# Performance work log

Measured on AMD Instinct MI355X. Metric: run time of the kernel, lower is better.

The kernel has to match this reference:

```python
import jax, jax.numpy as jnp
import numpy as np


def setup_inputs() -> dict:
    key = jax.random.key(0)
    k1, k2, k3, k4, k5 = jax.random.split(key, 5)
    N, L, H = 512, 512, 768
    num_texts = 32
    hidden_states = jax.random.normal(k1, (N, L, H), dtype=jnp.float32)
    attention_mask = jax.random.randint(k2, (N, L), 0, 2).astype(jnp.int32)
    sample_map = jnp.sort(jax.random.randint(k3, (N,), 0, num_texts).astype(jnp.int64))
    Wq = jax.random.normal(k4, (H, H), dtype=jnp.float32) * (1.0 / np.sqrt(H))
    bq = jnp.zeros((H,), dtype=jnp.float32)
    Wk = jax.random.normal(k5, (H, H), dtype=jnp.float32) * (1.0 / np.sqrt(H))
    bk = jnp.zeros((H,), dtype=jnp.float32)
    return {
        'hidden_states': hidden_states,
        'attention_mask': attention_mask,
        'sample_map': sample_map,
        'Wq': Wq, 'bq': bq, 'Wk': Wk, 'bk': bk,
        'num_texts': num_texts,
    }


def _attn_pool(hidden_states, mask, Wq, bq, Wk, bk):
    # hidden_states: [N, L, H]; mask: [N, L]
    H = hidden_states.shape[-1]
    # Q from mean over sequence (unmasked mean, as in original)
    q = jnp.einsum('nh,oh->no', hidden_states.mean(axis=1), Wq) + bq   # [N, H]
    k = jnp.einsum('nlh,oh->nlo', hidden_states, Wk) + bk              # [N, L, H]
    scores = jnp.einsum('nh,nlh->nl', q, k) / jnp.sqrt(jnp.float32(H))  # [N, L]
    scores = jnp.where(mask == 0, jnp.float32(-1e9), scores)
    alphas = jax.nn.softmax(scores, axis=1)                            # [N, L]
    return jnp.einsum('nl,nlh->nh', alphas, hidden_states)             # [N, H]


def reference(hidden_states, attention_mask, sample_map, Wq, bq, Wk, bk, num_texts):
    # dropout is identity in eval mode
    pooled = _attn_pool(hidden_states, attention_mask, Wq, bq, Wk, bk)  # [N, H]
    seg = sample_map.astype(jnp.int32)
    sums = jax.ops.segment_sum(pooled, seg, num_segments=num_texts)     # [T, H]
    counts = jax.ops.segment_sum(jnp.ones((pooled.shape[0],), pooled.dtype), seg,
                                 num_segments=num_texts)                # [T]
    counts = jnp.clip(counts, 1.0, None)
    return sums / counts[:, None]
```

## Files before the change

kernel.cpp:

```cpp
#include <hip/hip_runtime.h>
#include <math.h>

#define HDIM 768
#define NG   192
#define LMAX 512

__device__ __forceinline__ float dot4(const float4 a, const float4 b) {
  return a.x * b.x + a.y * b.y + a.z * b.z + a.w * b.w;
}
__device__ __forceinline__ void fma4(float4& a, const float s, const float4 b) {
  a.x += s * b.x; a.y += s * b.y; a.z += s * b.z; a.w += s * b.w;
}
__device__ __forceinline__ void scale4(float4& a, const float s) {
  a.x *= s; a.y *= s; a.z *= s; a.w *= s;
}

__device__ __forceinline__ float wave_sum64(float x) {
  x += __int_as_float(__builtin_amdgcn_update_dpp(0, __float_as_int(x), 0xB1,  0xF, 0xF, true));
  x += __int_as_float(__builtin_amdgcn_update_dpp(0, __float_as_int(x), 0x4E,  0xF, 0xF, true));
  x += __int_as_float(__builtin_amdgcn_update_dpp(0, __float_as_int(x), 0x124, 0xF, 0xF, true));
  x += __int_as_float(__builtin_amdgcn_update_dpp(0, __float_as_int(x), 0x128, 0xF, 0xF, true));
  x += __int_as_float(__builtin_amdgcn_update_dpp(0, __float_as_int(x), 0x142, 0xF, 0xF, true));
  x += __int_as_float(__builtin_amdgcn_update_dpp(0, __float_as_int(x), 0x143, 0xF, 0xF, true));
  return __int_as_float(__builtin_amdgcn_readlane(__float_as_int(x), 63));
}

__global__ __launch_bounds__(256) void detect_slots(const unsigned* __restrict__ mask_w,
                                                    const unsigned* __restrict__ smap_w,
                                                    unsigned* __restrict__ slots,
                                                    int mask_words, int smap_words) {
  __shared__ unsigned red[2];
  const int b = blockIdx.x, tid = threadIdx.x;
  if (tid < 2) red[tid] = 0;
  __syncthreads();
  const int gtid = b * 256 + tid, gsz = gridDim.x * 256;
  unsigned acc = 0;
  for (int i = gtid; i < mask_words / 2; i += gsz) acc |= mask_w[2 * i + 1];
  unsigned acc2 = 0;
  for (int i = gtid; i < smap_words / 2; i += gsz) acc2 |= smap_w[2 * i + 1];
  if (acc)  atomicOr(&red[0], 1u);
  if (acc2) atomicOr(&red[1], 1u);
  __syncthreads();
  if (tid == 0) { slots[b] = red[0]; slots[64 + b] = red[1]; }
}

__global__ __launch_bounds__(256) void prep_wc(const float* __restrict__ Wq,
                                               const float* __restrict__ Wk,
                                               const float* __restrict__ bq,
                                               float* __restrict__ Wc,
                                               float* __restrict__ c0, int H) {
  __shared__ float As[16][33];
  __shared__ float Bs[16][65];
  __shared__ float bqs[16];
  const int i0 = blockIdx.x * 32, j0 = blockIdx.y * 64;
  const int idx = threadIdx.x;
  const int li = idx & 31, lk = idx >> 5;
  const int lj = idx & 63, lk2 = idx >> 6;
  const int tc = idx & 15, tr = idx >> 4;
  float c[2][4] = {{0.f,0.f,0.f,0.f},{0.f,0.f,0.f,0.f}};
  float cb[4] = {0.f,0.f,0.f,0.f};
  const bool bias_lane = (blockIdx.x == 0) && (tr == 0);
  for (int o0 = 0; o0 < H; o0 += 16) {
    __syncthreads();
    As[lk][li]       = Wq[(size_t)(o0 + lk) * H + i0 + li];
    As[lk + 8][li]   = Wq[(size_t)(o0 + lk + 8) * H + i0 + li];
    Bs[lk2][lj]      = Wk[(size_t)(o0 + lk2) * H + j0 + lj];
    Bs[lk2 + 4][lj]  = Wk[(size_t)(o0 + lk2 + 4) * H + j0 + lj];
    Bs[lk2 + 8][lj]  = Wk[(size_t)(o0 + lk2 + 8) * H + j0 + lj];
    Bs[lk2 + 12][lj] = Wk[(size_t)(o0 + lk2 + 12) * H + j0 + lj];
    if (idx < 16) bqs[idx] = bq[o0 + idx];
    __syncthreads();
#pragma unroll
    for (int k = 0; k < 16; ++k) {
      const float a0 = As[k][tr * 2], a1 = As[k][tr * 2 + 1];
      const float b0 = Bs[k][tc * 4],     b1 = Bs[k][tc * 4 + 1];
      const float b2 = Bs[k][tc * 4 + 2], b3 = Bs[k][tc * 4 + 3];
      c[0][0] += a0 * b0; c[0][1] += a0 * b1; c[0][2] += a0 * b2; c[0][3] += a0 * b3;
      c[1][0] += a1 * b0; c[1][1] += a1 * b1; c[1][2] += a1 * b2; c[1][3] += a1 * b3;
      if (bias_lane) {
        const float bv = bqs[k];
        cb[0] += bv * b0; cb[1] += bv * b1; cb[2] += bv * b2; cb[3] += bv * b3;
      }
    }
  }
#pragma unroll
  for (int j = 0; j < 4; ++j) {
    Wc[(size_t)(i0 + tr * 2) * H + j0 + tc * 4 + j]     = c[0][j];
    Wc[(size_t)(i0 + tr * 2 + 1) * H + j0 + tc * 4 + j] = c[1][j];
  }
  if (bias_lane) {
#pragma unroll
    for (int j = 0; j < 4; ++j) c0[j0 + tc * 4 + j] = cb[j];
  }
}

__global__ __launch_bounds__(384) void fused(const float* __restrict__ hs,
                                             const unsigned* __restrict__ mask_w,
                                             const float* __restrict__ Wc,
                                             const float* __restrict__ c0,
                                             const unsigned* __restrict__ slots,
                                             float* __restrict__ pooled, int L) {
  __shared__ float4 red2[NG];
  __shared__ float4 meanv4[NG];
  __shared__ float4 vv4[NG];
  __shared__ float4 redv4[6][NG];
  __shared__ float mw[6], sw[6];
  __shared__ int   mrow[LMAX];
  __shared__ int   vidx[LMAX];
  __shared__ int   nv_sh;
  __shared__ unsigned mfl;
  const int n = blockIdx.x, tid = threadIdx.x;
  const int w = tid >> 6, lane = tid & 63;

  if (tid == 0) mfl = 0u;
  __syncthreads();
  if (tid < 64 && slots[tid]) atomicOr(&mfl, 1u);

  const int half = tid / NG, t = tid - half * NG;
  const float4* hb = reinterpret_cast<const float4*>(hs) + (size_t)n * L * NG;
  float ax = 0.f, ay = 0.f, az = 0.f, aw = 0.f;
  int l = half;
  for (; l + 16 <= L; l += 16) {
    float4 u[8];
#pragma unroll
    for (int i = 0; i < 8; ++i) u[i] = hb[(size_t)(l + 2 * i) * NG + t];
#pragma unroll
    for (int i = 0; i < 8; ++i) { ax += u[i].x; ay += u[i].y; az += u[i].z; aw += u[i].w; }
  }
  for (; l < L; l += 2) {
    float4 u = hb[(size_t)l * NG + t];
    ax += u.x; ay += u.y; az += u.z; aw += u.w;
  }
  if (half == 1) { float4 o; o.x = ax; o.y = ay; o.z = az; o.w = aw; red2[t] = o; }
  __syncthreads();

  if (half == 0) {
    const float inv = 1.0f / (float)L;
    const float4 r = red2[t];
    float4 o;
    o.x = (ax + r.x) * inv; o.y = (ay + r.y) * inv;
    o.z = (az + r.z) * inv; o.w = (aw + r.w) * inv;
    meanv4[t] = o;
  }
  const int mask_is_i32 = (mfl != 0);
  for (int tt = tid; tt < L; tt += 384) {
    const size_t idx = (size_t)n * L + tt;
    mrow[tt] = (int)(mask_is_i32 ? mask_w[idx] : mask_w[2 * idx]);
  }
  __syncthreads();

  if (w == 0) {
    int off = 0;
    for (int seg = 0; seg < L; seg += 64) {
      const int mv = mrow[seg + lane];
      const unsigned long long bal = __ballot(mv != 0);
      const int rank = __popcll(bal & ((1ull << lane) - 1ull));
      if (mv != 0) vidx[off + rank] = seg + lane;
      off += __popcll(bal);
    }
    if (lane == 0) nv_sh = off;
  }

  {
    const int c1 = tid, c2 = tid + 384;
    float acc1 = 0.f, acc2 = 0.f;
    const float* wp = Wc;
    for (int o = 0; o < HDIM; o += 4) {
      const float4 mv = meanv4[o >> 2];
      acc1 += mv.x * wp[c1] + mv.y * wp[HDIM + c1] + mv.z * wp[2 * HDIM + c1] + mv.w * wp[3 * HDIM + c1];
      acc2 += mv.x * wp[c2] + mv.y * wp[HDIM + c2] + mv.z * wp[2 * HDIM + c2] + mv.w * wp[3 * HDIM + c2];
      wp += 4 * HDIM;
    }
    ((float*)vv4)[c1] = acc1 + c0[c1];
    ((float*)vv4)[c2] = acc2 + c0[c2];
  }
  __syncthreads();

  const int nv = nv_sh;
  if (nv == 0) {
#pragma unroll
    for (int part = 0; part < 2; ++part) {
      const int col = part * 384 + tid;
      pooled[(size_t)n * HDIM + col] = ((const float*)meanv4)[col];
    }
    return;
  }

  const float4 vf0 = vv4[lane], vf1 = vv4[64 + lane], vf2 = vv4[128 + lane];
  const float scale = 1.0f / sqrtf((float)HDIM);
  const int cntw = (nv > w) ? ((nv - 1 - w) / 6 + 1) : 0;
  const int cmax = (nv + 5) / 6;
  const int jmax = (cmax + 3) & ~3;
  const int vidx0 = vidx[0];
  float m = -3.0e38f, ss = 0.f;
  float4 A0 = {0,0,0,0}, A1 = {0,0,0,0}, A2 = {0,0,0,0};
  float4 xa[2][3], xb[2][3];

  auto ld = [&](float4 (&X)[2][3], int j) {
#pragma unroll
    for (int u = 0; u < 2; ++u) {
      const int jj = j + u;
      const int rr = (jj < cntw) ? vidx[6 * jj + w] : vidx0;
      const float4* rp = hb + (size_t)rr * NG;
      X[u][0] = rp[lane]; X[u][1] = rp[64 + lane]; X[u][2] = rp[128 + lane];
    }
  };
  auto pr = [&](float4 (&X)[2][3], int j) {
    float s[2];
#pragma unroll
    for (int u = 0; u < 2; ++u) {
      const float p = wave_sum64(dot4(X[u][0], vf0) + dot4(X[u][1], vf1) + dot4(X[u][2], vf2));
      s[u] = (j + u < cntw) ? p * scale : -3.0e38f;
    }
    const float mc = fmaxf(s[0], s[1]);
    if (mc > m) {
      const float f = __expf(m - mc);
      ss *= f; scale4(A0, f); scale4(A1, f); scale4(A2, f);
      m = mc;
    }
#pragma unroll
    for (int u = 0; u < 2; ++u) {
      const float pq = (j + u < cntw) ? __expf(s[u] - m) : 0.f;
      ss += pq;
      fma4(A0, pq, X[u][0]); fma4(A1, pq, X[u][1]); fma4(A2, pq, X[u][2]);
    }
  };

  ld(xa, 0);
  for (int j = 0; j < jmax; j += 4) {
    ld(xb, j + 2);
    pr(xa, j);
    if (j + 4 < jmax) ld(xa, j + 4);
    pr(xb, j + 2);
  }

  if (lane == 0) { mw[w] = m; sw[w] = ss; }
  redv4[w][lane]       = A0;
  redv4[w][64 + lane]  = A1;
  redv4[w][128 + lane] = A2;
  __syncthreads();
  float M = mw[0];
#pragma unroll
  for (int j = 1; j < 6; ++j) M = fmaxf(M, mw[j]);
  float f[6], S = 0.f;
#pragma unroll
  for (int j = 0; j < 6; ++j) { f[j] = __expf(mw[j] - M); S += sw[j] * f[j]; }
  const float invS = 1.0f / S;
  const float* redp = (const float*)redv4;
#pragma unroll
  for (int part = 0; part < 2; ++part) {
    const int col = part * 384 + tid;
    float o = 0.f;
#pragma unroll
    for (int j = 0; j < 6; ++j) o += redp[j * HDIM + col] * f[j];
    pooled[(size_t)n * HDIM + col] = o * invS;
  }
}

__global__ __launch_bounds__(256) void segmean(const float* __restrict__ pooled,
                                               const void* __restrict__ smap,
                                               const unsigned* __restrict__ slots_s,
                                               float* __restrict__ out, int N) {
  __shared__ unsigned fsh;
  const int t = blockIdx.x, tid = threadIdx.x;
  const int col = blockIdx.y * 256 + tid;
  if (tid == 0) {
    unsigned f = 0;
    for (int i = 0; i < 64; ++i) f |= slots_s[i];
    fsh = f;
  }
  __syncthreads();
  const int smap_is_i32 = (fsh != 0);
  float a = 0.f;
  int cnt = 0;
  for (int i = 0; i < N; ++i) {
    const int s = smap_is_i32 ? ((const int*)smap)[i]
                              : (int)((const long long*)smap)[i];
    if (s == t) { a += pooled[(size_t)i * HDIM + col]; ++cnt; }
  }
  out[(size_t)t * HDIM + col] = a / (float)(cnt > 0 ? cnt : 1);
}

extern "C" void kernel_launch(void* const* d_in, const int* in_sizes, int n_in,
                              void* d_out, int out_size, void* d_ws, size_t ws_size,
                              hipStream_t stream) {
  const float*    hs     = (const float*)d_in[0];
  const unsigned* mask_w = (const unsigned*)d_in[1];
  const void*     smap   = d_in[2];
  const float*    Wq     = (const float*)d_in[3];
  const float*    bq     = (const float*)d_in[4];
  const float*    Wk     = (const float*)d_in[5];

  const int N = in_sizes[2];
  const int L = in_sizes[1] / N;
  const int H = in_sizes[4];
  const int T = out_size / H;

  float* Wc     = (float*)d_ws;
  float* c0     = Wc + (size_t)H * H;
  float* pooled = c0 + H;
  unsigned* slots = (unsigned*)(pooled + (size_t)N * H);
  (void)ws_size; (void)n_in;

  detect_slots<<<64, 256, 0, stream>>>(mask_w, (const unsigned*)smap, slots, N * L, N);
  prep_wc<<<dim3(H / 32, H / 64), 256, 0, stream>>>(Wq, Wk, bq, Wc, c0, H);
  fused<<<N, 384, 0, stream>>>(hs, mask_w, Wc, c0, slots, pooled, L);
  segmean<<<dim3(T, 3), 256, 0, stream>>>(pooled, smap, slots + 64, (float*)d_out, N);
}
```

Measured before the change: 367.6 us.

## Split fused pool into compacting pass, batched GEMV, and fp16 softmax pass

Replaces the single fused per-sample kernel with a multi-stage pipeline when workspace allows. The first pass reads hidden states once, computes partial means and writes the mask-compacted valid rows as fp16. A separate batched GEMM then forms query vectors for all samples, and a second pass runs the online softmax over the compacted fp16 rows, split in two halves per sample and merged in segmean. This aims to avoid re-reading full fp32 hidden states and to increase parallelism, at the cost of extra launches, extra workspace traffic and fp16 rounding error in the scores and pooled values. It silently falls back to the old path if the workspace is too small, and the RCAP=256 per-half capacity assumes L/2 ≤ 256.

```diff
diff --git a/kernel.cpp b/kernel.cpp
--- a/kernel.cpp
+++ b/kernel.cpp
@@ -1,9 +1,11 @@
 #include <hip/hip_runtime.h>
+#include <hip/hip_fp16.h>
 #include <math.h>
 
 #define HDIM 768
 #define NG   192
 #define LMAX 512
+#define RCAP 256
 
 __device__ __forceinline__ float dot4(const float4 a, const float4 b) {
   return a.x * b.x + a.y * b.y + a.z * b.z + a.w * b.w;
@@ -13,6 +15,12 @@
 }
 __device__ __forceinline__ void scale4(float4& a, const float s) {
   a.x *= s; a.y *= s; a.z *= s; a.w *= s;
+}
+__device__ __forceinline__ float4 h8_to_f4(uint2 v) {
+  __half2 h0 = *reinterpret_cast<__half2*>(&v.x);
+  __half2 h1 = *reinterpret_cast<__half2*>(&v.y);
+  const float2 f0 = __half22float2(h0), f1 = __half22float2(h1);
+  return make_float4(f0.x, f0.y, f1.x, f1.y);
 }
 
 __device__ __forceinline__ float wave_sum64(float x) {
@@ -94,6 +102,253 @@
   }
 }
 
+__global__ __launch_bounds__(384) void passA(const float* __restrict__ hs,
+                                             const unsigned* __restrict__ mask_w,
+                                             const unsigned* __restrict__ slots,
+                                             float* __restrict__ part,
+                                             int* __restrict__ nvalid,
+                                             __half* __restrict__ hsc, int L) {
+  __shared__ float4 red2[NG];
+  __shared__ int cpos[RCAP];
+  __shared__ int mrow[RCAP];
+  __shared__ unsigned mfl;
+  const int bid = blockIdx.x, n = bid >> 1, half = bid & 1;
+  const int tid = threadIdx.x, lane = tid & 63;
+  const int Lh = L / 2, r0 = half * Lh;
+
+  if (tid == 0) mfl = 0u;
+  __syncthreads();
+  if (tid < 64 && slots[tid]) atomicOr(&mfl, 1u);
+  __syncthreads();
+  const int m32 = (mfl != 0);
+  if (tid < Lh) {
+    const size_t idx = (size_t)n * L + r0 + tid;
+    mrow[tid] = (int)(m32 ? mask_w[idx] : mask_w[2 * idx]);
+  }
+  __syncthreads();
+
+  int nv = 0;
+  for (int seg = 0; seg < Lh; seg += 64) {
+    const int mv = mrow[seg + lane];
+    const unsigned long long bal = __ballot(mv != 0);
+    const int rank = __popcll(bal & ((1ull << lane) - 1ull));
+    cpos[seg + lane] = (mv != 0) ? (nv + rank) : -1;
+    nv += __popcll(bal);
+  }
+
+  const int sub = tid / NG, t = tid - sub * NG;
+  const float4* hb = reinterpret_cast<const float4*>(hs) + ((size_t)n * L + r0) * NG;
+  __half* reg = hsc + (size_t)bid * (RCAP * HDIM);
+  float ax = 0.f, ay = 0.f, az = 0.f, aw = 0.f;
+
+  auto st16 = [&](const float4 u, int cp) {
+    __half2 h0 = __floats2half2_rn(u.x, u.y);
+    __half2 h1 = __floats2half2_rn(u.z, u.w);
+    uint2 pk;
+    pk.x = *reinterpret_cast<unsigned*>(&h0);
+    pk.y = *reinterpret_cast<unsigned*>(&h1);
+    reinterpret_cast<uint2*>(reg + (size_t)cp * HDIM)[t] = pk;
+  };
+
+  int l = sub;
+  for (; l + 16 <= Lh; l += 16) {
+    float4 u[8];
+#pragma unroll
+    for (int i = 0; i < 8; ++i) u[i] = hb[(size_t)(l + 2 * i) * NG + t];
+#pragma unroll
+    for (int i = 0; i < 8; ++i) { ax += u[i].x; ay += u[i].y; az += u[i].z; aw += u[i].w; }
+#pragma unroll
+    for (int i = 0; i < 8; ++i) {
+      const int cp = cpos[l + 2 * i];
+      if (cp >= 0) st16(u[i], cp);
+    }
+  }
+  for (; l < Lh; l += 2) {
+    const float4 u = hb[(size_t)l * NG + t];
+    ax += u.x; ay += u.y; az += u.z; aw += u.w;
+    const int cp = cpos[l];
+    if (cp >= 0) st16(u, cp);
+  }
+
+  if (sub == 1) { float4 o; o.x = ax; o.y = ay; o.z = az; o.w = aw; red2[t] = o; }
+  __syncthreads();
+  if (sub == 0) {
+    const float4 r = red2[t];
+    float4 o; o.x = ax + r.x; o.y = ay + r.y; o.z = az + r.z; o.w = aw + r.w;
+    reinterpret_cast<float4*>(part + (size_t)bid * HDIM)[t] = o;
+  }
+  if (tid == 0) nvalid[bid] = nv;
+}
+
+__global__ __launch_bounds__(256) void gemmV(const float* __restrict__ P,
+                                             const float* __restrict__ Wc,
+                                             const float* __restrict__ c0,
+                                             float* __restrict__ V,
+                                             int M, int Nn, int K, float invL) {
+  __shared__ float As[32][17];
+  __shared__ float Bs[16][65];
+  const int m0 = blockIdx.x * 32, n0 = blockIdx.y * 64;
+  const int idx = threadIdx.x;
+  const int lc = idx & 15, lr = idx >> 4;
+  const int bc = idx & 63, br = idx >> 6;
+  const int tc = idx & 15, tr = idx >> 4;
+  float c[2][4] = {{0.f,0.f,0.f,0.f},{0.f,0.f,0.f,0.f}};
+  for (int k0 = 0; k0 < K; k0 += 16) {
+    __syncthreads();
+    {
+      const int m1 = m0 + lr, m2 = m0 + lr + 16;
+      As[lr][lc]      = (P[(size_t)(2 * m1) * K + k0 + lc] + P[(size_t)(2 * m1 + 1) * K + k0 + lc]) * invL;
+      As[lr + 16][lc] = (P[(size_t)(2 * m2) * K + k0 + lc] + P[(size_t)(2 * m2 + 1) * K + k0 + lc]) * invL;
+    }
+    Bs[br][bc]      = Wc[(size_t)(k0 + br) * Nn + n0 + bc];
+    Bs[br + 4][bc]  = Wc[(size_t)(k0 + br + 4) * Nn + n0 + bc];
+    Bs[br + 8][bc]  = Wc[(size_t)(k0 + br + 8) * Nn + n0 + bc];
+    Bs[br + 12][bc] = Wc[(size_t)(k0 + br + 12) * Nn + n0 + bc];
+    __syncthreads();
+#pragma unroll
+    for (int k = 0; k < 16; ++k) {
+      const float a0 = As[tr * 2][k], a1 = As[tr * 2 + 1][k];
+      const float b0 = Bs[k][tc * 4], b1 = Bs[k][tc * 4 + 1];
+      const float b2 = Bs[k][tc * 4 + 2], b3 = Bs[k][tc * 4 + 3];
+      c[0][0] += a0 * b0; c[0][1] += a0 * b1; c[0][2] += a0 * b2; c[0][3] += a0 * b3;
+      c[1][0] += a1 * b0; c[1][1] += a1 * b1; c[1][2] += a1 * b2; c[1][3] += a1 * b3;
+    }
+  }
+#pragma unroll
+  for (int j = 0; j < 4; ++j) {
+    const float bv = c0[n0 + tc * 4 + j];
+    V[(size_t)(m0 + tr * 2) * Nn + n0 + tc * 4 + j]     = c[0][j] + bv;
+    V[(size_t)(m0 + tr * 2 + 1) * Nn + n0 + tc * 4 + j] = c[1][j] + bv;
+  }
+}
+
+__global__ __launch_bounds__(256) void poolc(const __half* __restrict__ hsc,
+                                             const int* __restrict__ nvalid,
+                                             const float* __restrict__ part,
+                                             const float* __restrict__ V,
+                                             float* __restrict__ acc_out,
+                                             float* __restrict__ ms_out, int L) {
+  __shared__ float4 redv[4][NG];
+  __shared__ float mw[4], sw[4];
+  const int bid = blockIdx.x, n = bid >> 1;
+  const int tid = threadIdx.x, w = tid >> 6, lane = tid & 63;
+  const int Lh = L / 2;
+  const int nv = nvalid[bid];
+
+  if (nv == 0) {
+#pragma unroll
+    for (int p = 0; p < 3; ++p) {
+      const int col = p * 256 + tid;
+      acc_out[(size_t)bid * HDIM + col] = part[(size_t)bid * HDIM + col];
+    }
+    if (tid == 0) { ms_out[bid * 2] = -1e9f; ms_out[bid * 2 + 1] = (float)Lh; }
+    return;
+  }
+
+  const float4* v4 = reinterpret_cast<const float4*>(V + (size_t)n * HDIM);
+  const float4 vf0 = v4[lane], vf1 = v4[64 + lane], vf2 = v4[128 + lane];
+  const uint2* rb = reinterpret_cast<const uint2*>(hsc + (size_t)bid * (RCAP * HDIM));
+  const float scale = 1.0f / sqrtf((float)HDIM);
+
+  const int cntw = (nv > w) ? ((nv - 1 - w) / 4 + 1) : 0;
+  const int cmax = (nv + 3) / 4;
+  const int jmax = (cmax + 3) & ~3;
+  float m = -3.0e38f, ss = 0.f;
+  float4 A0 = {0,0,0,0}, A1 = {0,0,0,0}, A2 = {0,0,0,0};
+  uint2 xa[2][3], xb[2][3];
+
+  auto ld = [&](uint2 (&X)[2][3], int j) {
+#pragma unroll
+    for (int u = 0; u < 2; ++u) {
+      const int jj = j + u;
+      const int rr = (jj < cntw) ? (4 * jj + w) : 0;
+      const uint2* rp = rb + (size_t)rr * NG;
+      X[u][0] = rp[lane]; X[u][1] = rp[64 + lane]; X[u][2] = rp[128 + lane];
+    }
+  };
+  auto pr = [&](uint2 (&X)[2][3], int j) {
+    float4 y[2][3];
+    float s[2];
+#pragma unroll
+    for (int u = 0; u < 2; ++u) {
+      y[u][0] = h8_to_f4(X[u][0]); y[u][1] = h8_to_f4(X[u][1]); y[u][2] = h8_to_f4(X[u][2]);
+      const float p = wave_sum64(dot4(y[u][0], vf0) + dot4(y[u][1], vf1) + dot4(y[u][2], vf2));
+      s[u] = (j + u < cntw) ? p * scale : -3.0e38f;
+    }
+    const float mc = fmaxf(s[0], s[1]);
+    if (mc > m) {
+      const float f = __expf(m - mc);
+      ss *= f; scale4(A0, f); scale4(A1, f); scale4(A2, f);
+      m = mc;
+    }
+#pragma unroll
+    for (int u = 0; u < 2; ++u) {
+      const float pq = (j + u < cntw) ? __expf(s[u] - m) : 0.f;
+      ss += pq;
+      fma4(A0, pq, y[u][0]); fma4(A1, pq, y[u][1]); fma4(A2, pq, y[u][2]);
+    }
+  };
+
+  ld(xa, 0);
+  for (int j = 0; j < jmax; j += 4) {
+    ld(xb, j + 2);
+    pr(xa, j);
+    if (j + 4 < jmax) ld(xa, j + 4);
+    pr(xb, j + 2);
+  }
+
+  if (lane == 0) { mw[w] = m; sw[w] = ss; }
+  redv[w][lane]       = A0;
+  redv[w][64 + lane]  = A1;
+  redv[w][128 + lane] = A2;
+  __syncthreads();
+  const float M = fmaxf(fmaxf(mw[0], mw[1]), fmaxf(mw[2], mw[3]));
+  const float f0 = __expf(mw[0] - M), f1 = __expf(mw[1] - M);
+  const float f2 = __expf(mw[2] - M), f3 = __expf(mw[3] - M);
+  const float S = sw[0] * f0 + sw[1] * f1 + sw[2] * f2 + sw[3] * f3;
+  const float* redp = (const float*)redv;
+#pragma unroll
+  for (int p = 0; p < 3; ++p) {
+    const int col = p * 256 + tid;
+    acc_out[(size_t)bid * HDIM + col] =
+        redp[col] * f0 + redp[HDIM + col] * f1 + redp[2 * HDIM + col] * f2 + redp[3 * HDIM + col] * f3;
+  }
+  if (tid == 0) { ms_out[bid * 2] = M; ms_out[bid * 2 + 1] = S; }
+}
+
+__global__ __launch_bounds__(256) void merge_segmean(const float* __restrict__ acc,
+                                                     const float* __restrict__ ms,
+                                                     const void* __restrict__ smap,
+                                                     const unsigned* __restrict__ slots_s,
+                                                     float* __restrict__ out, int N) {
+  __shared__ unsigned fsh;
+  const int t = blockIdx.x, tid = threadIdx.x;
+  const int col = blockIdx.y * 256 + tid;
+  if (tid == 0) {
+    unsigned f = 0;
+    for (int i = 0; i < 64; ++i) f |= slots_s[i];
+    fsh = f;
+  }
+  __syncthreads();
+  const int smap_is_i32 = (fsh != 0);
+  float a = 0.f;
+  int cnt = 0;
+  for (int i = 0; i < N; ++i) {
+    const int s = smap_is_i32 ? ((const int*)smap)[i]
+                              : (int)((const long long*)smap)[i];
+    if (s != t) continue;
+    const float m0 = ms[(i * 2) * 2],     q0 = ms[(i * 2) * 2 + 1];
+    const float m1 = ms[(i * 2 + 1) * 2], q1 = ms[(i * 2 + 1) * 2 + 1];
+    const float M = fmaxf(m0, m1);
+    const float f0 = __expf(m0 - M), f1 = __expf(m1 - M);
+    const float S = q0 * f0 + q1 * f1;
+    const float o = (acc[(size_t)(i * 2) * HDIM + col] * f0 +
+                     acc[(size_t)(i * 2 + 1) * HDIM + col] * f1) / S;
+    a += o; ++cnt;
+  }
+  out[(size_t)t * HDIM + col] = a / (float)(cnt > 0 ? cnt : 1);
+}
+
 __global__ __launch_bounds__(384) void fused(const float* __restrict__ hs,
                                              const unsigned* __restrict__ mask_w,
                                              const float* __restrict__ Wc,
@@ -295,15 +550,41 @@
   const int L = in_sizes[1] / N;
   const int H = in_sizes[4];
   const int T = out_size / H;
-
-  float* Wc     = (float*)d_ws;
-  float* c0     = Wc + (size_t)H * H;
-  float* pooled = c0 + H;
-  unsigned* slots = (unsigned*)(pooled + (size_t)N * H);
-  (void)ws_size; (void)n_in;
-
-  detect_slots<<<64, 256, 0, stream>>>(mask_w, (const unsigned*)smap, slots, N * L, N);
-  prep_wc<<<dim3(H / 32, H / 64), 256, 0, stream>>>(Wq, Wk, bq, Wc, c0, H);
-  fused<<<N, 384, 0, stream>>>(hs, mask_w, Wc, c0, slots, pooled, L);
-  segmean<<<dim3(T, 3), 256, 0, stream>>>(pooled, smap, slots + 64, (float*)d_out, N);
-}
+  const size_t NH = (size_t)N * H;
+  (void)n_in;
+
+  const size_t f_words = (size_t)H * H + H + 2 * NH + NH + 2 * NH + 4 * N;
+  const size_t i_bytes = (128 + 2 * (size_t)N) * 4;
+  size_t hsc_off = (f_words * 4 + i_bytes + 255) & ~(size_t)255;
+  const size_t hsc_bytes = (size_t)2 * N * RCAP * H * 2;
+  const bool big = (ws_size >= hsc_off + hsc_bytes);
+
+  if (big) {
+    float* Wc   = (float*)d_ws;
+    float* c0   = Wc + (size_t)H * H;
+    float* part = c0 + H;
+    float* V    = part + 2 * NH;
+    float* acc  = V + NH;
+    float* ms   = acc + 2 * NH;
+    unsigned* slots = (unsigned*)(ms + 4 * N);
+    int* nvalid = (int*)(slots + 128);
+    __half* hsc = (__half*)((char*)d_ws + hsc_off);
+
+    detect_slots<<<64, 256, 0, stream>>>(mask_w, (const unsigned*)smap, slots, N * L, N);
+    prep_wc<<<dim3(H / 32, H / 64), 256, 0, stream>>>(Wq, Wk, bq, Wc, c0, H);
+    passA<<<2 * N, 384, 0, stream>>>(hs, mask_w, slots, part, nvalid, hsc, L);
+    gemmV<<<dim3(N / 32, H / 64), 256, 0, stream>>>(part, Wc, c0, V, N, H, H, 1.0f / (float)L);
+    poolc<<<2 * N, 256, 0, stream>>>(hsc, nvalid, part, V, acc, ms, L);
+    merge_segmean<<<dim3(T, 3), 256, 0, stream>>>(acc, ms, smap, slots + 64, (float*)d_out, N);
+  } else {
+    float* Wc     = (float*)d_ws;
+    float* c0     = Wc + (size_t)H * H;
+    float* pooled = c0 + H;
+    unsigned* slots = (unsigned*)(pooled + NH);
+
+    detect_slots<<<64, 256, 0, stream>>>(mask_w, (const unsigned*)smap, slots, N * L, N);
+    prep_wc<<<dim3(H / 32, H / 64), 256, 0, stream>>>(Wq, Wk, bq, Wc, c0, H);
+    fused<<<N, 384, 0, stream>>>(hs, mask_w, Wc, c0, slots, pooled, L);
+    segmean<<<dim3(T, 3), 256, 0, stream>>>(pooled, smap, slots + 64, (float*)d_out, N);
+  }
+}
```

After: 446.6 us. 21.5% more time.
